# Optimization experiments

Measured on AMD Instinct MI355X. Metric: run time of the kernel, lower is better.

The kernel has to match this reference:

```python
import jax, jax.numpy as jnp
import numpy as np

H, KVH, DH = 32, 8, 128        # attention heads, kv heads, head dim (shared by both streams)
G = H // KVH                   # GQA group size
EPS = 1e-6


def rms_norm(x, w):
    xf = x.astype(jnp.float32)
    n = xf * jax.lax.rsqrt(jnp.mean(xf * xf, axis=-1, keepdims=True) + EPS)
    return (n * w).astype(x.dtype)


def apply_rope(x, positions, max_wavelength=10000.0):
    # x: [B, L, h, DH], positions: [B, L]
    d_half = x.shape[-1] // 2
    freq_exponents = (2.0 / x.shape[-1]) * jnp.arange(d_half, dtype=jnp.float32)
    timescale = max_wavelength ** freq_exponents
    radians = positions[..., None].astype(jnp.float32) / timescale          # [B, L, d_half]
    radians = radians[..., None, :]                                         # [B, L, 1, d_half]
    s, c = jnp.sin(radians), jnp.cos(radians)
    xf = x.astype(jnp.float32)
    x1, x2 = xf[..., :d_half], xf[..., d_half:]
    out = jnp.concatenate([x1 * c - x2 * s, x2 * c + x1 * s], axis=-1)
    return out.astype(x.dtype)


def setup_inputs() -> dict:
    key = jax.random.key(0)
    ks = jax.random.split(key, 16)
    B, LV, LE = 2, 1024, 64
    DV, DE = 2560, 1920
    s = 0.02
    inp = {
        "vlm_embeds": jax.random.normal(ks[0], (B, LV, DV), jnp.float32),
        "expert_embeds": jax.random.normal(ks[1], (B, LE, DE), jnp.float32),
        "position_ids": jnp.sort(jax.random.randint(ks[2], (B, LV + LE), 0, 2048), axis=-1),
        "attention_mask": jnp.ones((B, LV + LE, LV + LE), dtype=bool),
        "w_ln_vlm": jnp.ones((DV,), jnp.float32),
        "Wq_vlm": jax.random.normal(ks[3], (DV, H * DH), jnp.float32) * s,
        "Wk_vlm": jax.random.normal(ks[4], (DV, KVH * DH), jnp.float32) * s,
        "Wv_vlm": jax.random.normal(ks[5], (DV, KVH * DH), jnp.float32) * s,
        "Wo_vlm": jax.random.normal(ks[6], (H * DH, DV), jnp.float32) * s,
        "w_ln_exp": jnp.ones((DE,), jnp.float32),
        "Wq_exp": jax.random.normal(ks[7], (DE, H * DH), jnp.float32) * s,
        "Wk_exp": jax.random.normal(ks[8], (DE, KVH * DH), jnp.float32) * s,
        "Wv_exp": jax.random.normal(ks[9], (DE, KVH * DH), jnp.float32) * s,
        "Wo_exp": jax.random.normal(ks[10], (H * DH, DE), jnp.float32) * s,
    }
    return inp


def _mixed_attn_layer(vlm_embeds, expert_embeds,
                      w_ln_vlm, Wq_vlm, Wk_vlm, Wv_vlm, Wo_vlm,
                      w_ln_exp, Wq_exp, Wk_exp, Wv_exp, Wo_exp,
                      position_ids, attention_mask, knowledge_insulation=True):
    B, LV, _ = vlm_embeds.shape
    LE = expert_embeds.shape[1]

    # Stream 0: VLM prefix (knowledge insulation -> no grad into VLM path).
    hv = rms_norm(vlm_embeds, w_ln_vlm)
    qv = (hv @ Wq_vlm).reshape(B, LV, H, DH)
    kv = (hv @ Wk_vlm).reshape(B, LV, KVH, DH)
    vv = (hv @ Wv_vlm).reshape(B, LV, KVH, DH)
    if knowledge_insulation:
        qv = jax.lax.stop_gradient(qv)
        kv = jax.lax.stop_gradient(kv)
        vv = jax.lax.stop_gradient(vv)

    # Stream 1: expert suffix.
    he = rms_norm(expert_embeds, w_ln_exp)
    qe = (he @ Wq_exp).reshape(B, LE, H, DH)
    ke = (he @ Wk_exp).reshape(B, LE, KVH, DH)
    ve = (he @ Wv_exp).reshape(B, LE, KVH, DH)

    # Concatenate streams along the sequence dim, then inline RoPE on q and k.
    q = jnp.concatenate([qv, qe], axis=1)          # [B, L, 32, 128]
    k = jnp.concatenate([kv, ke], axis=1)          # [B, L, 8, 128]
    v = jnp.concatenate([vv, ve], axis=1)
    q = apply_rope(q, position_ids)
    k = apply_rope(k, position_ids)

    # Eager GQA attention in fp32 (matches _eager_attention_forward).
    k_full = jnp.repeat(k, G, axis=2)              # kv-head major, group minor
    v_full = jnp.repeat(v, G, axis=2)
    att = jnp.einsum("bqhd,bkhd->bhqk", q.astype(jnp.float32), k_full.astype(jnp.float32))
    att = att * (DH ** -0.5)
    big_neg = jnp.finfo(jnp.float32).min
    att = jnp.where(attention_mask[:, None, :, :], att, big_neg)
    probs = jax.nn.softmax(att, axis=-1).astype(v_full.dtype)
    out = jnp.einsum("bhqk,bkhd->bqhd", probs, v_full).reshape(B, LV + LE, H * DH)

    # Split back to streams, per-stream output projection + residual.
    out_vlm = vlm_embeds + out[:, :LV] @ Wo_vlm
    out_exp = expert_embeds + out[:, LV:] @ Wo_exp
    return out_vlm, out_exp


def reference(vlm_embeds, expert_embeds, position_ids, attention_mask,
              w_ln_vlm, Wq_vlm, Wk_vlm, Wv_vlm, Wo_vlm,
              w_ln_exp, Wq_exp, Wk_exp, Wv_exp, Wo_exp):
    _, out_exp = _mixed_attn_layer(
        vlm_embeds, expert_embeds,
        w_ln_vlm, Wq_vlm, Wk_vlm, Wv_vlm, Wo_vlm,
        w_ln_exp, Wq_exp, Wk_exp, Wv_exp, Wo_exp,
        position_ids, attention_mask)
    return out_exp
```

## Files before the change

### kernel.cpp

```cpp
#include <hip/hip_runtime.h>
#include <hip/hip_bf16.h>
#include <cstddef>

#define B_  2
#define LV_ 1024
#define LE_ 64
#define S_TOT 1088
#define DV_ 2560
#define DE_ 1920
#define H_  32
#define KVH_ 8
#define DH_ 128
#define HD_ 4096
#define KVD_ 1024
#define NSPL 9

typedef short short8 __attribute__((ext_vector_type(8)));
typedef float f32x4 __attribute__((ext_vector_type(4)));

typedef __hip_bfloat16 bf16;

__device__ inline float b2f(bf16 h) { return __bfloat162float(h); }
__device__ inline bf16 f2b(float f) { return __float2bfloat16(f); }

typedef const __attribute__((address_space(1))) void* gptr_t;
typedef __attribute__((address_space(3))) void* lptr_t;
__device__ inline void gl16(const void* g, void* l) {
  __builtin_amdgcn_global_load_lds((gptr_t)g, (lptr_t)l, 16, 0, 0);
}

#define OFF_HVB   0ul
#define OFF_WKVT  10485760ul
#define OFF_HEB   20971520ul
#define OFF_WQKVT 21463040ul
#define OFF_QE    45056000ul
#define OFF_KBUF  46104576ul
#define OFF_VBUF  50561024ul
#define OFF_AO    59473920ul
#define OFF_WOT   0ul
#define OFF_M     20971520ul
#define OFF_L     21118976ul
#define OFF_OP    21463040ul
#define OFF_P2    21463040ul

#define NSPLIT2 16

__global__ __launch_bounds__(256) void rmsnorm_bf16(
    const float* __restrict__ x, const float* __restrict__ w,
    bf16* __restrict__ out, int D) {
  int row = blockIdx.x;
  const float4* x4 = (const float4*)(x + (size_t)row * D);
  const float4* w4 = (const float4*)w;
  int D4 = D >> 2;
  float ss = 0.f;
  for (int i = threadIdx.x; i < D4; i += 256) {
    float4 v = x4[i];
    ss += v.x * v.x + v.y * v.y + v.z * v.z + v.w * v.w;
  }
  __shared__ float red[256];
  red[threadIdx.x] = ss; __syncthreads();
  for (int s = 128; s > 0; s >>= 1) {
    if (threadIdx.x < s) red[threadIdx.x] += red[threadIdx.x + s];
    __syncthreads();
  }
  float inv = rsqrtf(red[0] / (float)D + 1e-6f);
  ushort4* o4 = (ushort4*)(out + (size_t)row * D);
  for (int i = threadIdx.x; i < D4; i += 256) {
    float4 v = x4[i], wv = w4[i];
    bf16 a = f2b(v.x * inv * wv.x), b = f2b(v.y * inv * wv.y);
    bf16 c = f2b(v.z * inv * wv.z), d = f2b(v.w * inv * wv.w);
    ushort4 o;
    o.x = *(ushort*)&a; o.y = *(ushort*)&b; o.z = *(ushort*)&c; o.w = *(ushort*)&d;
    o4[i] = o;
  }
}

__device__ inline void tile_tconv(float (*t)[65],
    const float* __restrict__ W, bf16* __restrict__ Wt,
    int K, int N, int n_off, int bx, int by) {
  int n0 = bx * 64, k0 = by * 64;
  int tid = threadIdx.x;
  int c = tid & 63, r4 = tid >> 6;
#pragma unroll 4
  for (int it = 0; it < 16; ++it) {
    int k = it * 4 + r4;
    t[k][c] = W[(size_t)(k0 + k) * N + n0 + c];
  }
  __syncthreads();
#pragma unroll 4
  for (int it = 0; it < 16; ++it) {
    int n = it * 4 + r4;
    Wt[(size_t)(n_off + n0 + n) * K + k0 + c] = f2b(t[c][n]);
  }
}

__global__ __launch_bounds__(256) void tconv(
    const float* __restrict__ W, bf16* __restrict__ Wt,
    int K, int N, int n_off) {
  __shared__ float t[64][65];
  tile_tconv(t, W, Wt, K, N, n_off, blockIdx.x, blockIdx.y);
}

__global__ __launch_bounds__(256) void tconv_all(
    const float* __restrict__ Wk_vlm, const float* __restrict__ Wv_vlm,
    const float* __restrict__ Wq_exp, const float* __restrict__ Wk_exp,
    const float* __restrict__ Wv_exp,
    bf16* __restrict__ WkvT, bf16* __restrict__ WqkvT) {
  __shared__ float t[64][65];
  int id = blockIdx.x;
  if (id < 640)       tile_tconv(t, Wk_vlm, WkvT, DV_, KVD_, 0,    id % 16, id / 16);
  else if (id < 1280) { id -= 640;  tile_tconv(t, Wv_vlm, WkvT,  DV_, KVD_, 1024, id % 16, id / 16); }
  else if (id < 3200) { id -= 1280; tile_tconv(t, Wq_exp, WqkvT, DE_, HD_,  0,    id % 64, id / 64); }
  else if (id < 3680) { id -= 3200; tile_tconv(t, Wk_exp, WqkvT, DE_, KVD_, 4096, id % 16, id / 16); }
  else                { id -= 3680; tile_tconv(t, Wv_exp, WqkvT, DE_, KVD_, 5120, id % 16, id / 16); }
}

__global__ __launch_bounds__(256) void gemm_fused(
    const bf16* __restrict__ hv, const bf16* __restrict__ WkvT,
    const bf16* __restrict__ he, const bf16* __restrict__ WqkvT,
    bf16* __restrict__ kbuf, bf16* __restrict__ vbuf, bf16* __restrict__ qe) {
  __shared__ ushort As[3][128][32];
  __shared__ ushort Bs[3][128][32];
  int tid = threadIdx.x;
  int lane = tid & 63, w = tid >> 6;
  int lr = lane & 15, quad = lane >> 4;
  int wm = (w >> 1) * 64, wn = (w & 1) * 64;

  bool expert = (blockIdx.x >= 256);
  const ushort* Ab; const ushort* Bb; int K, nsteps, m0, n0;
  if (!expert) {
    m0 = (blockIdx.x >> 4) * 128; n0 = (blockIdx.x & 15) * 128;
    Ab = (const ushort*)hv; Bb = (const ushort*)WkvT;
    K = DV_; nsteps = DV_ / 32;
  } else {
    m0 = 0; n0 = (int)(blockIdx.x - 256) * 128;
    Ab = (const ushort*)he; Bb = (const ushort*)WqkvT;
    K = DE_; nsteps = DE_ / 32;
  }

  int r0 = w * 32 + (lane >> 2);
  int r1 = r0 + 16;
  int s0 = (lane & 3) ^ ((r0 >> 1) & 3);
  int s1 = (lane & 3) ^ ((r1 >> 1) & 3);
  const ushort* sa0 = Ab + (size_t)(m0 + r0) * K + s0 * 8;
  const ushort* sa1 = Ab + (size_t)(m0 + r1) * K + s1 * 8;
  const ushort* sb0 = Bb + (size_t)(n0 + r0) * K + s0 * 8;
  const ushort* sb1 = Bb + (size_t)(n0 + r1) * K + s1 * 8;

  auto STAGE = [&](int buf, int t) {
    int k0 = t * 32;
    gl16(sa0 + k0, &As[buf][w * 32][0]);
    gl16(sb0 + k0, &Bs[buf][w * 32][0]);
    gl16(sa1 + k0, &As[buf][w * 32 + 16][0]);
    gl16(sb1 + k0, &Bs[buf][w * 32 + 16][0]);
  };

  int sslot = (quad ^ ((lr >> 1) & 3)) * 8;

  f32x4 acc[4][4] = {};

  STAGE(0, 0);
  STAGE(1, 1);
  int cur = 0, nxt = 2;
  for (int t = 0; t < nsteps; ++t) {
    if (t + 2 < nsteps) {
      STAGE(nxt, t + 2);
      asm volatile("s_waitcnt vmcnt(8)" ::: "memory");
    } else if (t + 2 == nsteps) {
      asm volatile("s_waitcnt vmcnt(4)" ::: "memory");
    } else {
      asm volatile("s_waitcnt vmcnt(0)" ::: "memory");
    }
    __builtin_amdgcn_s_barrier();

    short8 af[4], bv[4];
#pragma unroll
    for (int i = 0; i < 4; ++i) {
      af[i] = *(const short8*)&As[cur][wm + i * 16 + lr][sslot];
      bv[i] = *(const short8*)&Bs[cur][wn + i * 16 + lr][sslot];
    }
#pragma unroll
    for (int i = 0; i < 4; ++i)
#pragma unroll
      for (int j = 0; j < 4; ++j)
        acc[i][j] = __builtin_amdgcn_mfma_f32_16x16x32_bf16(af[i], bv[j], acc[i][j], 0, 0, 0);

    __builtin_amdgcn_s_barrier();
    cur = (cur == 2) ? 0 : cur + 1;
    nxt = (nxt == 2) ? 0 : nxt + 1;
  }

#pragma unroll
  for (int i = 0; i < 4; ++i) {
    int mm_base = wm + i * 16 + quad * 4;
#pragma unroll
    for (int j = 0; j < 4; ++j) {
      int gn = n0 + wn + j * 16 + lr;
#pragma unroll
      for (int r = 0; r < 4; ++r) {
        int mm = mm_base + r;
        float v = acc[i][j][r];
        if (!expert) {
          int m = m0 + mm;
          int b = m >> 10, s = m & 1023;
          size_t row = (size_t)(b * S_TOT + s);
          if (gn < 1024) kbuf[row * KVD_ + gn] = f2b(v);
          else           vbuf[row * KVD_ + (gn - 1024)] = f2b(v);
        } else {
          int b = mm >> 6, l = mm & 63;
          if (gn < 4096) {
            qe[(size_t)mm * HD_ + gn] = f2b(v);
          } else {
            size_t row = (size_t)(b * S_TOT + LV_ + l);
            if (gn < 5120) kbuf[row * KVD_ + (gn - 4096)] = f2b(v);
            else           vbuf[row * KVD_ + (gn - 5120)] = f2b(v);
          }
        }
      }
    }
  }
}

__global__ __launch_bounds__(256) void gemm_splitk(
    const bf16* __restrict__ A, const bf16* __restrict__ Bt,
    int N, int K_full, int Kc, float* __restrict__ partial) {
  __shared__ ushort As[128][40];
  __shared__ ushort Bs[64][40];
  int tid = threadIdx.x;
  int lane = tid & 63, wid = tid >> 6;
  int wm = (wid >> 1) * 64, wn = (wid & 1) * 32;
  int n0 = blockIdx.x * 64;
  int k_beg = blockIdx.y * Kc, k_end = k_beg + Kc;
  int lrow = lane & 15, quad = lane >> 4;

  f32x4 acc[4][2] = {};

  int ar = tid >> 2;
  int ac = (tid & 3) * 8;
  const ushort* Aptr = (const ushort*)A + (size_t)ar * K_full + ac;
  const ushort* Bptr = (const ushort*)Bt + (size_t)(n0 + ar) * K_full + ac;

  for (int k0 = k_beg; k0 < k_end; k0 += 32) {
    short8 a0 = *(const short8*)(Aptr + k0);
    short8 a1 = *(const short8*)(Aptr + (size_t)64 * K_full + k0);
    short8 b0 = *(const short8*)(Bptr + k0);
    __syncthreads();
    *(short8*)&As[ar][ac] = a0;
    *(short8*)&As[64 + ar][ac] = a1;
    *(short8*)&Bs[ar][ac] = b0;
    __syncthreads();
    short8 af[4], bfr[2];
#pragma unroll
    for (int i = 0; i < 4; ++i)
      af[i]  = *(const short8*)&As[wm + i * 16 + lrow][quad * 8];
#pragma unroll
    for (int j = 0; j < 2; ++j)
      bfr[j] = *(const short8*)&Bs[wn + j * 16 + lrow][quad * 8];
#pragma unroll
    for (int i = 0; i < 4; ++i)
#pragma unroll
      for (int j = 0; j < 2; ++j)
        acc[i][j] = __builtin_amdgcn_mfma_f32_16x16x32_bf16(af[i], bfr[j], acc[i][j], 0, 0, 0);
  }

  float* pbase = partial + (size_t)blockIdx.y * 128 * N;
#pragma unroll
  for (int i = 0; i < 4; ++i) {
    int m_base = wm + i * 16 + quad * 4;
#pragma unroll
    for (int j = 0; j < 2; ++j) {
      int gn = n0 + wn + j * 16 + lrow;
#pragma unroll
      for (int r = 0; r < 4; ++r)
        pbase[(size_t)(m_base + r) * N + gn] = acc[i][j][r];
    }
  }
}

__global__ __launch_bounds__(256) void reduce_out(
    const float* __restrict__ partial, const float* __restrict__ residual,
    float* __restrict__ out) {
  int idx = (blockIdx.x * 256 + threadIdx.x) * 4;
  f32x4 s = *(const f32x4*)(residual + idx);
#pragma unroll
  for (int sp = 0; sp < NSPLIT2; ++sp) {
    const f32x4 v = *(const f32x4*)(partial + (size_t)sp * 128 * 1920 + idx);
    s += v;
  }
  *(f32x4*)(out + idx) = s;
}

__global__ __launch_bounds__(256) void rope_fused(
    bf16* __restrict__ qe, bf16* __restrict__ kbuf,
    const int* __restrict__ pos_ids) {
  if (blockIdx.x < 128) {
    int row = blockIdx.x;
    int b = row >> 6, l = row & 63;
    float pos = (float)pos_ids[b * S_TOT + LV_ + l];
    bf16* qrow = qe + (size_t)row * HD_;
    for (int p = threadIdx.x; p < H_ * 64; p += 256) {
      int hh = p >> 6, i = p & 63;
      float inv_ts = expf(-9.210340371976184f * (float)i * (1.0f / 64.0f));
      float r = pos * inv_ts;
      float sn = sinf(r), cs = cosf(r);
      float x1 = b2f(qrow[hh * DH_ + i]), x2 = b2f(qrow[hh * DH_ + i + 64]);
      qrow[hh * DH_ + i]      = f2b(x1 * cs - x2 * sn);
      qrow[hh * DH_ + i + 64] = f2b(x2 * cs + x1 * sn);
    }
  } else {
    int bid = blockIdx.x - 128;
    int s = bid % S_TOT, b = bid / S_TOT;
    float pos = (float)pos_ids[b * S_TOT + s];
    size_t base = ((size_t)(b * S_TOT + s)) * KVD_;
    for (int t = threadIdx.x; t < KVH_ * 64; t += 256) {
      int kvh = t >> 6, i = t & 63;
      size_t idx = base + kvh * DH_ + i;
      float inv_ts = expf(-9.210340371976184f * (float)i * (1.0f / 64.0f));
      float r = pos * inv_ts;
      float sn = sinf(r), cs = cosf(r);
      float x1 = b2f(kbuf[idx]), x2 = b2f(kbuf[idx + 64]);
      kbuf[idx]      = f2b(x1 * cs - x2 * sn);
      kbuf[idx + 64] = f2b(x2 * cs + x1 * sn);
    }
  }
}

__global__ __launch_bounds__(256) void attn_part(
    const bf16* __restrict__ qe, const bf16* __restrict__ kbuf,
    const bf16* __restrict__ vbuf,
    float* __restrict__ O_p, float* __restrict__ m_arr,
    float* __restrict__ l_arr) {
  int bh = blockIdx.x & 63;
  int split = blockIdx.x >> 6;
  int h = bh & 31, b = bh >> 5;
  int kvh = h >> 2;
  int tid = threadIdx.x;
  int lane = tid & 63, wid = tid >> 6;
  int lr = lane & 15, quad = lane >> 4;

  __shared__ ushort Ks[64][152];
  __shared__ ushort vTs[128][72];
  __shared__ ushort sc[4][16][72];

  short8 qf[4];
  {
    const ushort* qptr = (const ushort*)qe +
        ((size_t)(b * LE_ + wid * 16 + lr)) * HD_ + h * DH_ + quad * 8;
#pragma unroll
    for (int ks = 0; ks < 4; ++ks) qf[ks] = *(const short8*)(qptr + ks * 32);
  }

  f32x4 Of[8] = {};
  float m_i[4], l_i[4];
#pragma unroll
  for (int r = 0; r < 4; ++r) { m_i[r] = -1e30f; l_i[r] = 0.f; }

  const float scale = 0.08838834764831845f;
  int nch = (split == 8) ? 1 : 2;

  for (int c = 0; c < nch; ++c) {
    int key0 = split * 128 + c * 64;
    __syncthreads();
    {
      int dg = tid & 15, kq = tid >> 4;
#pragma unroll
      for (int it = 0; it < 4; ++it) {
        int key = it * 16 + kq;
        short8 v = *(const short8*)((const ushort*)kbuf +
            ((size_t)(b * S_TOT + key0 + key) * KVH_ + kvh) * DH_ + dg * 8);
        *(short8*)&Ks[key][dg * 8] = v;
      }
    }
    {
      int key = tid & 63, dgrp = tid >> 6;
      const ushort* vp = (const ushort*)vbuf +
          ((size_t)(b * S_TOT + key0 + key) * KVH_ + kvh) * DH_ + dgrp * 32;
      short8 vv[4];
#pragma unroll
      for (int q8 = 0; q8 < 4; ++q8) vv[q8] = *(const short8*)(vp + q8 * 8);
#pragma unroll
      for (int q8 = 0; q8 < 4; ++q8)
#pragma unroll
        for (int j = 0; j < 8; ++j)
          vTs[dgrp * 32 + q8 * 8 + j][key] = (ushort)vv[q8][j];
    }
    __syncthreads();

    f32x4 Sf[4] = {};
#pragma unroll
    for (int kt = 0; kt < 4; ++kt)
#pragma unroll
      for (int ks = 0; ks < 4; ++ks) {
        short8 kf = *(const short8*)&Ks[kt * 16 + lr][quad * 8 + ks * 32];
        Sf[kt] = __builtin_amdgcn_mfma_f32_16x16x32_bf16(qf[ks], kf, Sf[kt], 0, 0, 0);
      }

#pragma unroll
    for (int kt = 0; kt < 4; ++kt) Sf[kt] *= scale;
#pragma unroll
    for (int r = 0; r < 4; ++r) {
      float mx = fmaxf(fmaxf(Sf[0][r], Sf[1][r]), fmaxf(Sf[2][r], Sf[3][r]));
#pragma unroll
      for (int msk = 1; msk < 16; msk <<= 1) mx = fmaxf(mx, __shfl_xor(mx, msk));
      float mn = fmaxf(m_i[r], mx);
      float alpha = __expf(m_i[r] - mn);
      m_i[r] = mn;
      float ls = 0.f;
#pragma unroll
      for (int kt = 0; kt < 4; ++kt) {
        float p = __expf(Sf[kt][r] - mn);
        Sf[kt][r] = p;
        ls += p;
      }
      l_i[r] = l_i[r] * alpha + ls;
#pragma unroll
      for (int nt = 0; nt < 8; ++nt) Of[nt][r] *= alpha;
#pragma unroll
      for (int kt = 0; kt < 4; ++kt) {
        bf16 t = f2b(Sf[kt][r]);
        sc[wid][quad * 4 + r][kt * 16 + lr] = *(ushort*)&t;
      }
    }

#pragma unroll
    for (int ks = 0; ks < 2; ++ks) {
      short8 pf = *(const short8*)&sc[wid][lr][quad * 8 + ks * 32];
#pragma unroll
      for (int nt = 0; nt < 8; ++nt) {
        short8 vf = *(const short8*)&vTs[nt * 16 + lr][quad * 8 + ks * 32];
        Of[nt] = __builtin_amdgcn_mfma_f32_16x16x32_bf16(pf, vf, Of[nt], 0, 0, 0);
      }
    }
  }

  float l_row[4];
#pragma unroll
  for (int r = 0; r < 4; ++r) {
    float l = l_i[r];
#pragma unroll
    for (int msk = 1; msk < 16; msk <<= 1) l += __shfl_xor(l, msk);
    l_row[r] = l;
  }

  size_t rbase = (size_t)split * 4096 + (size_t)bh * 64;
#pragma unroll
  for (int nt = 0; nt < 8; ++nt)
#pragma unroll
    for (int r = 0; r < 4; ++r) {
      int q = wid * 16 + quad * 4 + r;
      O_p[(rbase + q) * 128 + nt * 16 + lr] = Of[nt][r];
    }
  if (lr == 0) {
#pragma unroll
    for (int r = 0; r < 4; ++r) {
      int q = wid * 16 + quad * 4 + r;
      m_arr[rbase + q] = m_i[r];
      l_arr[rbase + q] = l_row[r];
    }
  }
}

__global__ __launch_bounds__(256) void attn_combine(
    const float* __restrict__ O_p, const float* __restrict__ m_arr,
    const float* __restrict__ l_arr, bf16* __restrict__ ao) {
  int t = blockIdx.x * 256 + threadIdx.x;
  int d = t & 127, row = t >> 7;
  float m_g = -1e30f;
#pragma unroll
  for (int s = 0; s < NSPL; ++s) m_g = fmaxf(m_g, m_arr[s * 4096 + row]);
  float denom = 0.f, acc = 0.f;
#pragma unroll
  for (int s = 0; s < NSPL; ++s) {
    float w = __expf(m_arr[s * 4096 + row] - m_g);
    denom += w * l_arr[s * 4096 + row];
    acc   += w * O_p[((size_t)s * 4096 + row) * 128 + d];
  }
  int b = row >> 11, h = (row >> 6) & 31, q = row & 63;
  bf16 o = f2b(acc / denom);
  ((ushort*)ao)[((size_t)(b * 64 + q) * 32 + h) * 128 + d] = *(ushort*)&o;
}

extern "C" void kernel_launch(void* const* d_in, const int* in_sizes, int n_in,
                              void* d_out, int out_size, void* d_ws, size_t ws_size,
                              hipStream_t stream) {
  const float* vlm      = (const float*)d_in[0];
  const float* expe     = (const float*)d_in[1];
  const int*   pos      = (const int*)d_in[2];
  const float* w_ln_vlm = (const float*)d_in[4];
  const float* Wk_vlm   = (const float*)d_in[6];
  const float* Wv_vlm   = (const float*)d_in[7];
  const float* w_ln_exp = (const float*)d_in[9];
  const float* Wq_exp   = (const float*)d_in[10];
  const float* Wk_exp   = (const float*)d_in[11];
  const float* Wv_exp   = (const float*)d_in[12];
  const float* Wo_exp   = (const float*)d_in[13];
  float* out = (float*)d_out;
  char* ws = (char*)d_ws;

  bf16* hv_b  = (bf16*)(ws + OFF_HVB);
  bf16* WkvT  = (bf16*)(ws + OFF_WKVT);
  bf16* he_b  = (bf16*)(ws + OFF_HEB);
  bf16* WqkvT = (bf16*)(ws + OFF_WQKVT);
  bf16* qe    = (bf16*)(ws + OFF_QE);
  bf16* kbuf  = (bf16*)(ws + OFF_KBUF);
  bf16* vbuf  = (bf16*)(ws + OFF_VBUF);
  bf16* ao    = (bf16*)(ws + OFF_AO);
  bf16* WoT   = (bf16*)(ws + OFF_WOT);
  float* m_arr = (float*)(ws + OFF_M);
  float* l_arr = (float*)(ws + OFF_L);
  float* O_p   = (float*)(ws + OFF_OP);
  float* part2 = (float*)(ws + OFF_P2);

  rmsnorm_bf16<<<B_ * LV_, 256, 0, stream>>>(vlm, w_ln_vlm, hv_b, DV_);
  rmsnorm_bf16<<<B_ * LE_, 256, 0, stream>>>(expe, w_ln_exp, he_b, DE_);

  tconv_all<<<4160, 256, 0, stream>>>(Wk_vlm, Wv_vlm, Wq_exp, Wk_exp, Wv_exp,
                                      WkvT, WqkvT);

  gemm_fused<<<304, 256, 0, stream>>>(hv_b, WkvT, he_b, WqkvT, kbuf, vbuf, qe);

  rope_fused<<<128 + B_ * S_TOT, 256, 0, stream>>>(qe, kbuf, pos);

  tconv<<<dim3(30, 64), 256, 0, stream>>>(Wo_exp, WoT, HD_, DE_, 0);

  attn_part<<<64 * NSPL, 256, 0, stream>>>(qe, kbuf, vbuf, O_p, m_arr, l_arr);
  attn_combine<<<4096 * 128 / 256, 256, 0, stream>>>(O_p, m_arr, l_arr, ao);

  gemm_splitk<<<dim3(30, NSPLIT2), 256, 0, stream>>>(ao, WoT, 1920, HD_,
                                                     HD_ / NSPLIT2, part2);
  reduce_out<<<128 * 1920 / 4 / 256, 256, 0, stream>>>(part2, expe, out);
}
```

Baseline: 317.8 us.

## Fuse Wo conversion into output GEMM, merge rmsnorms, deepen QKV GEMM pipeline

The output projection GEMM now reads fp32 Wo_exp directly, converts it to bf16 in registers and stores it transposed into swizzled LDS. This removes the separate transpose-convert kernel and its bf16 copy of Wo. The two rmsnorm launches are merged into one grid. The fused QKV GEMM moves from a 3-stage to a 4-stage LDS prefetch pipeline. In exchange, the output GEMM issues strided scalar fp32 loads of W, the QKV GEMM uses more LDS, and launch count drops.

```diff
diff --git a/kernel.cpp b/kernel.cpp
--- a/kernel.cpp
+++ b/kernel.cpp
@@ -37,7 +37,6 @@
 #define OFF_KBUF  46104576ul
 #define OFF_VBUF  50561024ul
 #define OFF_AO    59473920ul
-#define OFF_WOT   0ul
 #define OFF_M     20971520ul
 #define OFF_L     21118976ul
 #define OFF_OP    21463040ul
@@ -45,10 +44,14 @@
 
 #define NSPLIT2 16
 
-__global__ __launch_bounds__(256) void rmsnorm_bf16(
-    const float* __restrict__ x, const float* __restrict__ w,
-    bf16* __restrict__ out, int D) {
-  int row = blockIdx.x;
+__global__ __launch_bounds__(256) void rmsnorm_both(
+    const float* __restrict__ xv, const float* __restrict__ wv,
+    bf16* __restrict__ ov,
+    const float* __restrict__ xe, const float* __restrict__ we,
+    bf16* __restrict__ oe) {
+  int row; const float* x; const float* w; bf16* o; int D;
+  if (blockIdx.x < 2048) { row = blockIdx.x;        x = xv; w = wv; o = ov; D = DV_; }
+  else                   { row = blockIdx.x - 2048; x = xe; w = we; o = oe; D = DE_; }
   const float4* x4 = (const float4*)(x + (size_t)row * D);
   const float4* w4 = (const float4*)w;
   int D4 = D >> 2;
@@ -64,14 +67,14 @@
     __syncthreads();
   }
   float inv = rsqrtf(red[0] / (float)D + 1e-6f);
-  ushort4* o4 = (ushort4*)(out + (size_t)row * D);
+  ushort4* o4 = (ushort4*)(o + (size_t)row * D);
   for (int i = threadIdx.x; i < D4; i += 256) {
-    float4 v = x4[i], wv = w4[i];
-    bf16 a = f2b(v.x * inv * wv.x), b = f2b(v.y * inv * wv.y);
-    bf16 c = f2b(v.z * inv * wv.z), d = f2b(v.w * inv * wv.w);
-    ushort4 o;
-    o.x = *(ushort*)&a; o.y = *(ushort*)&b; o.z = *(ushort*)&c; o.w = *(ushort*)&d;
-    o4[i] = o;
+    float4 v = x4[i], wv2 = w4[i];
+    bf16 a = f2b(v.x * inv * wv2.x), b = f2b(v.y * inv * wv2.y);
+    bf16 c = f2b(v.z * inv * wv2.z), d = f2b(v.w * inv * wv2.w);
+    ushort4 ow;
+    ow.x = *(ushort*)&a; ow.y = *(ushort*)&b; ow.z = *(ushort*)&c; ow.w = *(ushort*)&d;
+    o4[i] = ow;
   }
 }
 
@@ -92,13 +95,6 @@
     int n = it * 4 + r4;
     Wt[(size_t)(n_off + n0 + n) * K + k0 + c] = f2b(t[c][n]);
   }
-}
-
-__global__ __launch_bounds__(256) void tconv(
-    const float* __restrict__ W, bf16* __restrict__ Wt,
-    int K, int N, int n_off) {
-  __shared__ float t[64][65];
-  tile_tconv(t, W, Wt, K, N, n_off, blockIdx.x, blockIdx.y);
 }
 
 __global__ __launch_bounds__(256) void tconv_all(
@@ -119,8 +115,8 @@
     const bf16* __restrict__ hv, const bf16* __restrict__ WkvT,
     const bf16* __restrict__ he, const bf16* __restrict__ WqkvT,
     bf16* __restrict__ kbuf, bf16* __restrict__ vbuf, bf16* __restrict__ qe) {
-  __shared__ ushort As[3][128][32];
-  __shared__ ushort Bs[3][128][32];
+  __shared__ ushort As[4][128][32];
+  __shared__ ushort Bs[4][128][32];
   int tid = threadIdx.x;
   int lane = tid & 63, w = tid >> 6;
   int lr = lane & 15, quad = lane >> 4;
@@ -161,18 +157,22 @@
 
   STAGE(0, 0);
   STAGE(1, 1);
-  int cur = 0, nxt = 2;
+  STAGE(2, 2);
   for (int t = 0; t < nsteps; ++t) {
-    if (t + 2 < nsteps) {
-      STAGE(nxt, t + 2);
+    int rem = nsteps - t;
+    if (rem > 3) {
+      STAGE((t + 3) & 3, t + 3);
+      asm volatile("s_waitcnt vmcnt(12)" ::: "memory");
+    } else if (rem == 3) {
       asm volatile("s_waitcnt vmcnt(8)" ::: "memory");
-    } else if (t + 2 == nsteps) {
+    } else if (rem == 2) {
       asm volatile("s_waitcnt vmcnt(4)" ::: "memory");
     } else {
       asm volatile("s_waitcnt vmcnt(0)" ::: "memory");
     }
     __builtin_amdgcn_s_barrier();
 
+    int cur = t & 3;
     short8 af[4], bv[4];
 #pragma unroll
     for (int i = 0; i < 4; ++i) {
@@ -186,8 +186,6 @@
         acc[i][j] = __builtin_amdgcn_mfma_f32_16x16x32_bf16(af[i], bv[j], acc[i][j], 0, 0, 0);
 
     __builtin_amdgcn_s_barrier();
-    cur = (cur == 2) ? 0 : cur + 1;
-    nxt = (nxt == 2) ? 0 : nxt + 1;
   }
 
 #pragma unroll
@@ -221,41 +219,49 @@
   }
 }
 
-__global__ __launch_bounds__(256) void gemm_splitk(
-    const bf16* __restrict__ A, const bf16* __restrict__ Bt,
-    int N, int K_full, int Kc, float* __restrict__ partial) {
+__global__ __launch_bounds__(256) void gemm_out(
+    const bf16* __restrict__ A, const float* __restrict__ W,
+    float* __restrict__ partial) {
   __shared__ ushort As[128][40];
   __shared__ ushort Bs[64][40];
   int tid = threadIdx.x;
   int lane = tid & 63, wid = tid >> 6;
   int wm = (wid >> 1) * 64, wn = (wid & 1) * 32;
   int n0 = blockIdx.x * 64;
-  int k_beg = blockIdx.y * Kc, k_end = k_beg + Kc;
-  int lrow = lane & 15, quad = lane >> 4;
+  int k_beg = blockIdx.y * 256;
+  int lr = lane & 15, quad = lane >> 4;
 
   f32x4 acc[4][2] = {};
 
   int ar = tid >> 2;
   int ac = (tid & 3) * 8;
-  const ushort* Aptr = (const ushort*)A + (size_t)ar * K_full + ac;
-  const ushort* Bptr = (const ushort*)Bt + (size_t)(n0 + ar) * K_full + ac;
-
-  for (int k0 = k_beg; k0 < k_end; k0 += 32) {
+  const ushort* Aptr = (const ushort*)A + (size_t)ar * HD_ + ac;
+  int bn = tid & 63, kg = tid >> 6;
+  int bslot_w = ((kg ^ (bn & 3)) * 8);
+  int brd = (quad ^ (lr & 3)) * 8;
+
+  for (int k0 = k_beg; k0 < k_beg + 256; k0 += 32) {
     short8 a0 = *(const short8*)(Aptr + k0);
-    short8 a1 = *(const short8*)(Aptr + (size_t)64 * K_full + k0);
-    short8 b0 = *(const short8*)(Bptr + k0);
+    short8 a1 = *(const short8*)(Aptr + (size_t)64 * HD_ + k0);
+    float wv[8];
+#pragma unroll
+    for (int j = 0; j < 8; ++j)
+      wv[j] = W[(size_t)(k0 + kg * 8 + j) * DE_ + n0 + bn];
+    short8 bvv;
+#pragma unroll
+    for (int j = 0; j < 8; ++j) { bf16 h = f2b(wv[j]); bvv[j] = *(short*)&h; }
     __syncthreads();
     *(short8*)&As[ar][ac] = a0;
     *(short8*)&As[64 + ar][ac] = a1;
-    *(short8*)&Bs[ar][ac] = b0;
+    *(short8*)&Bs[bn][bslot_w] = bvv;
     __syncthreads();
     short8 af[4], bfr[2];
 #pragma unroll
     for (int i = 0; i < 4; ++i)
-      af[i]  = *(const short8*)&As[wm + i * 16 + lrow][quad * 8];
+      af[i]  = *(const short8*)&As[wm + i * 16 + lr][quad * 8];
 #pragma unroll
     for (int j = 0; j < 2; ++j)
-      bfr[j] = *(const short8*)&Bs[wn + j * 16 + lrow][quad * 8];
+      bfr[j] = *(const short8*)&Bs[wn + j * 16 + lr][brd];
 #pragma unroll
     for (int i = 0; i < 4; ++i)
 #pragma unroll
@@ -263,16 +269,16 @@
         acc[i][j] = __builtin_amdgcn_mfma_f32_16x16x32_bf16(af[i], bfr[j], acc[i][j], 0, 0, 0);
   }
 
-  float* pbase = partial + (size_t)blockIdx.y * 128 * N;
+  float* pbase = partial + (size_t)blockIdx.y * 128 * 1920;
 #pragma unroll
   for (int i = 0; i < 4; ++i) {
     int m_base = wm + i * 16 + quad * 4;
 #pragma unroll
     for (int j = 0; j < 2; ++j) {
-      int gn = n0 + wn + j * 16 + lrow;
+      int gn = n0 + wn + j * 16 + lr;
 #pragma unroll
       for (int r = 0; r < 4; ++r)
-        pbase[(size_t)(m_base + r) * N + gn] = acc[i][j][r];
+        pbase[(size_t)(m_base + r) * 1920 + gn] = acc[i][j][r];
     }
   }
 }
@@ -505,14 +511,13 @@
   bf16* kbuf  = (bf16*)(ws + OFF_KBUF);
   bf16* vbuf  = (bf16*)(ws + OFF_VBUF);
   bf16* ao    = (bf16*)(ws + OFF_AO);
-  bf16* WoT   = (bf16*)(ws + OFF_WOT);
   float* m_arr = (float*)(ws + OFF_M);
   float* l_arr = (float*)(ws + OFF_L);
   float* O_p   = (float*)(ws + OFF_OP);
   float* part2 = (float*)(ws + OFF_P2);
 
-  rmsnorm_bf16<<<B_ * LV_, 256, 0, stream>>>(vlm, w_ln_vlm, hv_b, DV_);
-  rmsnorm_bf16<<<B_ * LE_, 256, 0, stream>>>(expe, w_ln_exp, he_b, DE_);
+  rmsnorm_both<<<B_ * LV_ + B_ * LE_, 256, 0, stream>>>(
+      vlm, w_ln_vlm, hv_b, expe, w_ln_exp, he_b);
 
   tconv_all<<<4160, 256, 0, stream>>>(Wk_vlm, Wv_vlm, Wq_exp, Wk_exp, Wv_exp,
                                       WkvT, WqkvT);
@@ -521,12 +526,9 @@
 
   rope_fused<<<128 + B_ * S_TOT, 256, 0, stream>>>(qe, kbuf, pos);
 
-  tconv<<<dim3(30, 64), 256, 0, stream>>>(Wo_exp, WoT, HD_, DE_, 0);
-
   attn_part<<<64 * NSPL, 256, 0, stream>>>(qe, kbuf, vbuf, O_p, m_arr, l_arr);
   attn_combine<<<4096 * 128 / 256, 256, 0, stream>>>(O_p, m_arr, l_arr, ao);
 
-  gemm_splitk<<<dim3(30, NSPLIT2), 256, 0, stream>>>(ao, WoT, 1920, HD_,
-                                                     HD_ / NSPLIT2, part2);
+  gemm_out<<<dim3(30, NSPLIT2), 256, 0, stream>>>(ao, Wo_exp, part2);
   reduce_out<<<128 * 1920 / 4 / 256, 256, 0, stream>>>(part2, expe, out);
 }
```

After: 306.6 us. 3.5% less time.
